# Kernel optimization log

Hardware: AMD Instinct MI355X
Metric: run time of the kernel (lower is better)

The kernel has to match this reference:

```python
import jax, jax.numpy as jnp
import numpy as np

S = 1024      # graphs (frames / LSTM seq_len)
NPG = 64      # nodes per graph
N = S * NPG   # total nodes
E = 524288    # total edges (512 per graph)
NF, EF = 32, 16
HC = 64       # hidden_channels
H1 = 3        # gat1 heads
NEG_SLOPE = 0.2


def _p(k, shape):
    return 0.1 * jax.random.normal(k, shape, dtype=jnp.float32)


def setup_inputs():
    key = jax.random.key(0)
    ks = jax.random.split(key, 30)
    x = jax.random.normal(ks[0], (N, NF), jnp.float32)
    local = jax.random.randint(ks[1], (2, E), 0, NPG)
    off = jnp.repeat(jnp.arange(S) * NPG, E // S)  # edges grouped per graph
    edge_index = local + off[None, :]
    edge_attr = jax.random.normal(ks[2], (E, EF), jnp.float32)
    batch = jnp.repeat(jnp.arange(S), NPG)
    return {
        'x': x, 'edge_index': edge_index, 'edge_attr': edge_attr, 'batch': batch,
        # gat1: in=NF, out=HC, heads=H1, edge_dim=EF
        'Wl1': _p(ks[3], (NF, H1 * HC)), 'bl1': _p(ks[4], (H1 * HC,)),
        'Wr1': _p(ks[5], (NF, H1 * HC)), 'br1': _p(ks[6], (H1 * HC,)),
        'We1': _p(ks[7], (EF, H1 * HC)), 'att1': _p(ks[8], (H1, HC)),
        'bias1': _p(ks[9], (H1 * HC,)),
        # gat2: in=H1*HC, out=HC, heads=1
        'Wl2': _p(ks[10], (H1 * HC, HC)), 'bl2': _p(ks[11], (HC,)),
        'Wr2': _p(ks[12], (H1 * HC, HC)), 'br2': _p(ks[13], (HC,)),
        'We2': _p(ks[14], (EF, HC)), 'att2': _p(ks[15], (1, HC)),
        'bias2': _p(ks[16], (HC,)),
        # LSTM (torch gate order i,f,g,o)
        'Wih': _p(ks[17], (4 * HC, HC)), 'Whh': _p(ks[18], (4 * HC, HC)),
        'bih': _p(ks[19], (4 * HC,)), 'bhh': _p(ks[20], (4 * HC,)),
        # MLP head
        'W1': _p(ks[21], (HC, HC // 2)), 'b1': _p(ks[22], (HC // 2,)),
        'W2': _p(ks[23], (HC // 2, 1)), 'b2': _p(ks[24], (1,)),
    }


def gatv2(x, edge_index, edge_attr, Wl, bl, Wr, br, We, att, bias, H, C):
    n = x.shape[0]
    src, dst = edge_index[0], edge_index[1]
    # add self loops, edge_attr filled with per-target mean (PyG fill_value='mean')
    deg = jax.ops.segment_sum(jnp.ones((edge_attr.shape[0],), x.dtype), dst, num_segments=n)
    loop_attr = jax.ops.segment_sum(edge_attr, dst, num_segments=n) / jnp.maximum(deg, 1.0)[:, None]
    ar = jnp.arange(n)
    src_f = jnp.concatenate([src, ar])
    dst_f = jnp.concatenate([dst, ar])
    ea_f = jnp.concatenate([edge_attr, loop_attr], axis=0)
    xl = (x @ Wl + bl).reshape(n, H, C)   # source-side transform (message carrier)
    xr = (x @ Wr + br).reshape(n, H, C)   # target-side transform
    eproj = (ea_f @ We).reshape(-1, H, C)
    m = jax.nn.leaky_relu(xl[src_f] + xr[dst_f] + eproj, NEG_SLOPE)  # [Ef,H,C]
    score = jnp.einsum('ehc,hc->eh', m, att)
    smax = jax.ops.segment_max(score, dst_f, num_segments=n)
    expv = jnp.exp(score - smax[dst_f])
    denom = jax.ops.segment_sum(expv, dst_f, num_segments=n)
    alpha = expv / (denom[dst_f] + 1e-16)
    out = jax.ops.segment_sum(alpha[..., None] * xl[src_f], dst_f, num_segments=n)
    return out.reshape(n, H * C) + bias


def lstm_last_hidden(seq, Wih, Whh, bih, bhh):
    # seq: [S, HC]; torch LSTM single layer, h0=c0=0
    def step(carry, xt):
        h, c = carry
        g = Wih @ xt + Whh @ h + bih + bhh
        i, f, gg, o = jnp.split(g, 4)
        c = jax.nn.sigmoid(f) * c + jax.nn.sigmoid(i) * jnp.tanh(gg)
        h = jax.nn.sigmoid(o) * jnp.tanh(c)
        return (h, c), None
    (h, c), _ = jax.lax.scan(step, (jnp.zeros((HC,), seq.dtype), jnp.zeros((HC,), seq.dtype)), seq)
    return h


def reference(x, edge_index, edge_attr, batch, Wl1, bl1, Wr1, br1, We1, att1, bias1,
              Wl2, bl2, Wr2, br2, We2, att2, bias2, Wih, Whh, bih, bhh, W1, b1, W2, b2):
    h = jax.nn.elu(gatv2(x, edge_index, edge_attr, Wl1, bl1, Wr1, br1, We1, att1, bias1, H1, HC))
    h = jax.nn.elu(gatv2(h, edge_index, edge_attr, Wl2, bl2, Wr2, br2, We2, att2, bias2, 1, HC))
    cnt = jax.ops.segment_sum(jnp.ones((N, 1), h.dtype), batch, num_segments=S)
    pooled = jax.ops.segment_sum(h, batch, num_segments=S) / cnt  # [S, HC]
    last = lstm_last_hidden(pooled, Wih, Whh, bih, bhh)[None, :]  # [1, HC]; dropout is identity in eval
    out = jax.nn.relu(last @ W1 + b1) @ W2 + b2  # [1, 1]
    return out
```

## Files before the change

### kernel.cpp

```cpp
#include <hip/hip_runtime.h>

#define ETOT 524288
#define SGR  1024
#define NPG  64
#define EPG  512
#define NFD  32
#define EFD  16
#define HCD  64

typedef float f2v __attribute__((ext_vector_type(2)));

__device__ __forceinline__ float elu_(float x){ return x>0.f ? x : (__expf(x)-1.f); }
__device__ __forceinline__ float sig_(float x){ return 1.f/(1.f+__expf(-x)); }
__device__ __forceinline__ float tanhf_(float x){ float e=__expf(2.f*x); return 1.f-2.f/(e+1.f); }
__device__ __forceinline__ float lrelu_(float x){ return x>0.f ? x : 0.2f*x; }

template<int C>
__device__ __forceinline__ float dppf(float v){
  return __int_as_float(__builtin_amdgcn_update_dpp(0, __float_as_int(v), C, 0xF, 0xF, true));
}

__device__ __forceinline__ float quad_add(float v){
  v += dppf<0xB1>(v);
  return v + dppf<0x4E>(v);
}

__device__ void build_csr_la(int tid, int g, const int* ei, const float* ea,
                             int* s_edge, int* s_entry, int* s_off, int* s_deg,
                             int* s_cnt, float* s_la)
{
  const int base = g*NPG;
  const int* srcp = ei + (size_t)g*EPG;
  const int* dstp = ei + (size_t)ETOT + (size_t)g*EPG;
  s_edge[tid] = (srcp[tid]-base) | ((dstp[tid]-base)<<6);
  __syncthreads();
  { const int d=tid>>3, s=tid&7, b0=s*64;
    int c=0;
    #pragma unroll 8
    for(int i=0;i<64;i++) c += (((s_edge[b0+i]>>6)&63)==d);
    s_cnt[(d<<3)|s]=c; }
  __syncthreads();
  if(tid<64){ int a=0;
    #pragma unroll
    for(int s=0;s<8;s++) a+=s_cnt[(tid<<3)|s];
    s_deg[tid]=a; }
  __syncthreads();
  if(tid==0){ int a=0;
    for(int i=0;i<64;i++){ s_off[i]=a; a+=s_deg[i]; }
    s_off[64]=a; }
  __syncthreads();
  { const int d=tid>>3, s=tid&7, b0=s*64;
    int pos=s_off[d];
    for(int s2=0;s2<s;s2++) pos += s_cnt[(d<<3)|s2];
    for(int i=0;i<64;i++){ int en=s_edge[b0+i];
      if(((en>>6)&63)==d) s_entry[pos++] = (en&63) | (d<<6) | ((b0+i)<<12); } }
  __syncthreads();
  if(tid<256){ int n=tid>>2, f0=(tid&3)*4;
    float a0=0,a1=0,a2=0,a3=0;
    const int b=s_off[n], en=s_off[n+1];
    for(int p=b;p<en;p++){ int eid=s_entry[p]>>12;
      const float4 v = *(const float4*)(ea + ((size_t)g*EPG+(size_t)eid)*EFD + f0);
      a0+=v.x; a1+=v.y; a2+=v.z; a3+=v.w; }
    float inv = 1.f/fmaxf((float)(en-b),1.f);
    float4 r; r.x=a0*inv; r.y=a1*inv; r.z=a2*inv; r.w=a3*inv;
    *(float4*)(s_la + n*EFD + f0) = r; }
  __syncthreads();
}

__device__ void scores_softmax(int tid, int g, const float* ea,
   const int* s_entry, const int* s_off, const float* s_la,
   const float* s_We, const float* s_att, const float* s_xl, const float* s_xr,
   float* s_sc)
{
  for(int p=tid;p<576;p+=512){
    int src,dst; float eav[16];
    if(p<EPG){
      int en=s_entry[p]; src=en&63; dst=(en>>6)&63; int eid=en>>12;
      const float* epp = ea + ((size_t)g*EPG + (size_t)eid)*EFD;
      float4 v0=*(const float4*)(epp),   v1=*(const float4*)(epp+4);
      float4 v2=*(const float4*)(epp+8), v3=*(const float4*)(epp+12);
      eav[0]=v0.x;eav[1]=v0.y;eav[2]=v0.z;eav[3]=v0.w;
      eav[4]=v1.x;eav[5]=v1.y;eav[6]=v1.z;eav[7]=v1.w;
      eav[8]=v2.x;eav[9]=v2.y;eav[10]=v2.z;eav[11]=v2.w;
      eav[12]=v3.x;eav[13]=v3.y;eav[14]=v3.z;eav[15]=v3.w;
    } else {
      int n=p-EPG; src=n; dst=n;
      const float* epp = s_la + n*EFD;
      float4 v0=*(const float4*)(epp),   v1=*(const float4*)(epp+4);
      float4 v2=*(const float4*)(epp+8), v3=*(const float4*)(epp+12);
      eav[0]=v0.x;eav[1]=v0.y;eav[2]=v0.z;eav[3]=v0.w;
      eav[4]=v1.x;eav[5]=v1.y;eav[6]=v1.z;eav[7]=v1.w;
      eav[8]=v2.x;eav[9]=v2.y;eav[10]=v2.z;eav[11]=v2.w;
      eav[12]=v3.x;eav[13]=v3.y;eav[14]=v3.z;eav[15]=v3.w;
    }
    float score=0.f;
    #pragma unroll 4
    for(int cq=0;cq<16;cq++){
      float e0=0.f,e1=0.f,e2=0.f,e3=0.f;
      #pragma unroll
      for(int f=0;f<16;f++){
        const float4 wv=*(const float4*)(s_We + f*64 + cq*4);
        e0+=eav[f]*wv.x; e1+=eav[f]*wv.y; e2+=eav[f]*wv.z; e3+=eav[f]*wv.w;
      }
      const float4 xlv=*(const float4*)(s_xl + src*64 + ((cq^(src&15))<<2));
      const float4 xrv=*(const float4*)(s_xr + dst*64 + ((cq^(dst&15))<<2));
      const float4 av =*(const float4*)(s_att + cq*4);
      float m0=lrelu_(xlv.x+xrv.x+e0), m1=lrelu_(xlv.y+xrv.y+e1);
      float m2=lrelu_(xlv.z+xrv.z+e2), m3=lrelu_(xlv.w+xrv.w+e3);
      score += m0*av.x+m1*av.y+m2*av.z+m3*av.w;
    }
    s_sc[p]=score;
  }
  __syncthreads();
  { const int d=tid>>3, s=tid&7;
    const int b=s_off[d], e=s_off[d+1];
    float mx=-1e30f;
    for(int p=b+s;p<e;p+=8) mx=fmaxf(mx,s_sc[p]);
    if(s==0) mx=fmaxf(mx,s_sc[EPG+d]);
    mx=fmaxf(mx,dppf<0xB1>(mx));
    mx=fmaxf(mx,dppf<0x4E>(mx));
    mx=fmaxf(mx,dppf<0x141>(mx));
    float den=0.f;
    for(int p=b+s;p<e;p+=8){ float w=__expf(s_sc[p]-mx); s_sc[p]=w; den+=w; }
    float selfv=0.f;
    if(s==0){ selfv=__expf(s_sc[EPG+d]-mx); den+=selfv; }
    den+=dppf<0xB1>(den);
    den+=dppf<0x4E>(den);
    den+=dppf<0x141>(den);
    const float inv=1.f/(den+1e-16f);
    for(int p=b+s;p<e;p+=8) s_sc[p]*=inv;
    if(s==0) s_sc[EPG+d]=selfv*inv;
  }
  __syncthreads();
}

__global__ __launch_bounds__(512,4) void gat1_k(
    const float* __restrict__ x, const int* __restrict__ ei,
    const float* __restrict__ ea, const float* __restrict__ Wl,
    const float* __restrict__ bl, const float* __restrict__ Wr,
    const float* __restrict__ br, const float* __restrict__ We,
    const float* __restrict__ att, const float* __restrict__ bias,
    float* __restrict__ h1)
{
  const int g = blockIdx.x, tid = threadIdx.x;
  const int base = g*NPG;

  __shared__ __align__(16) float s_x[NPG*36];
  __shared__ __align__(16) float s_xl[NPG*64];
  __shared__ __align__(16) float s_xr[NPG*64];
  __shared__ __align__(16) float s_W[2*32*64];
  __shared__ __align__(16) float s_We[16*64];
  __shared__ __align__(16) float s_att[64];
  __shared__ __align__(16) float s_la[NPG*EFD];
  __shared__ float s_sc[576];
  __shared__ int   s_edge[EPG];
  __shared__ int   s_entry[EPG];
  __shared__ int   s_cnt[512];
  __shared__ int   s_off[65];
  __shared__ int   s_deg[64];

  { int n=tid>>3, kq=tid&7;
    float4 v = *(const float4*)(x + (size_t)(base+n)*NFD + kq*4);
    *(float4*)(s_x + n*36 + kq*4) = v; }

  build_csr_la(tid, g, ei, ea, s_edge, s_entry, s_off, s_deg, s_cnt, s_la);

  for(int h=0;h<3;h++){
    { int k=tid>>4, c0=(tid&15)*4;
      *(float4*)(s_W + k*64 + c0)        = *(const float4*)(Wl + (size_t)k*192 + h*64 + c0);
      *(float4*)(s_W + 2048 + k*64 + c0) = *(const float4*)(Wr + (size_t)k*192 + h*64 + c0); }
    if(tid<256){ int f=tid>>4, c0=(tid&15)*4;
      *(float4*)(s_We + f*64 + c0) = *(const float4*)(We + (size_t)f*192 + h*64 + c0); }
    if(tid<16) *(float4*)(s_att + tid*4) = *(const float4*)(att + h*64 + tid*4);
    __syncthreads();

    { const int cg=tid&15, ng=tid>>4, n0=ng*2, c0=cg*4;
      const float4 blv=*(const float4*)(bl + h*64 + c0);
      const float4 brv=*(const float4*)(br + h*64 + c0);
      float accl[2][4]={{blv.x,blv.y,blv.z,blv.w},{blv.x,blv.y,blv.z,blv.w}};
      float accr[2][4]={{brv.x,brv.y,brv.z,brv.w},{brv.x,brv.y,brv.z,brv.w}};
      #pragma unroll
      for(int kq=0;kq<8;kq++){
        float xs0[4], xs1[4];
        { float4 v=*(const float4*)(s_x + n0*36 + kq*4);     xs0[0]=v.x;xs0[1]=v.y;xs0[2]=v.z;xs0[3]=v.w; }
        { float4 v=*(const float4*)(s_x + (n0+1)*36 + kq*4); xs1[0]=v.x;xs1[1]=v.y;xs1[2]=v.z;xs1[3]=v.w; }
        #pragma unroll
        for(int f=0;f<4;f++){
          const float4 wl=*(const float4*)(s_W + (kq*4+f)*64 + c0);
          const float4 wr=*(const float4*)(s_W + 2048 + (kq*4+f)*64 + c0);
          accl[0][0]+=xs0[f]*wl.x; accl[0][1]+=xs0[f]*wl.y; accl[0][2]+=xs0[f]*wl.z; accl[0][3]+=xs0[f]*wl.w;
          accl[1][0]+=xs1[f]*wl.x; accl[1][1]+=xs1[f]*wl.y; accl[1][2]+=xs1[f]*wl.z; accl[1][3]+=xs1[f]*wl.w;
          accr[0][0]+=xs0[f]*wr.x; accr[0][1]+=xs0[f]*wr.y; accr[0][2]+=xs0[f]*wr.z; accr[0][3]+=xs0[f]*wr.w;
          accr[1][0]+=xs1[f]*wr.x; accr[1][1]+=xs1[f]*wr.y; accr[1][2]+=xs1[f]*wr.z; accr[1][3]+=xs1[f]*wr.w;
        }
      }
      #pragma unroll
      for(int i=0;i<2;i++){
        const int n=n0+i, sq=((cg^(n&15))<<2);
        float4 vl; vl.x=accl[i][0]; vl.y=accl[i][1]; vl.z=accl[i][2]; vl.w=accl[i][3];
        float4 vr; vr.x=accr[i][0]; vr.y=accr[i][1]; vr.z=accr[i][2]; vr.w=accr[i][3];
        *(float4*)(s_xl + n*64 + sq)=vl;
        *(float4*)(s_xr + n*64 + sq)=vr;
      }
    }
    __syncthreads();

    scores_softmax(tid, g, ea, s_entry, s_off, s_la, s_We, s_att, s_xl, s_xr, s_sc);

    { const int n=tid>>3, c0a=(tid&7)*8;
      float acc[8]={0.f,0.f,0.f,0.f,0.f,0.f,0.f,0.f};
      const int b=s_off[n], e=s_off[n+1];
      for(int p=b;p<e;p++){
        const int en=s_entry[p], src=en&63;
        const float a=s_sc[p];
        #pragma unroll
        for(int qq=0;qq<2;qq++){
          const int cq=(c0a>>2)+qq;
          const float4 xv=*(const float4*)(s_xl + src*64 + ((cq^(src&15))<<2));
          acc[qq*4+0]+=a*xv.x; acc[qq*4+1]+=a*xv.y; acc[qq*4+2]+=a*xv.z; acc[qq*4+3]+=a*xv.w;
        }
      }
      { const float a=s_sc[EPG+n];
        #pragma unroll
        for(int qq=0;qq<2;qq++){
          const int cq=(c0a>>2)+qq;
          const float4 xv=*(const float4*)(s_xl + n*64 + ((cq^(n&15))<<2));
          acc[qq*4+0]+=a*xv.x; acc[qq*4+1]+=a*xv.y; acc[qq*4+2]+=a*xv.z; acc[qq*4+3]+=a*xv.w;
        } }
      float* op = h1 + (size_t)(base+n)*192 + h*64 + c0a;
      #pragma unroll
      for(int qq=0;qq<2;qq++){
        const float4 bv=*(const float4*)(bias + h*64 + c0a + qq*4);
        float4 r; r.x=elu_(acc[qq*4+0]+bv.x); r.y=elu_(acc[qq*4+1]+bv.y);
                  r.z=elu_(acc[qq*4+2]+bv.z); r.w=elu_(acc[qq*4+3]+bv.w);
        *(float4*)(op + qq*4)=r;
      }
    }
    __syncthreads();
  }
}

__global__ __launch_bounds__(512,4) void gat2_k(
    const float* __restrict__ h1, const int* __restrict__ ei,
    const float* __restrict__ ea, const float* __restrict__ Wl,
    const float* __restrict__ bl, const float* __restrict__ Wr,
    const float* __restrict__ br, const float* __restrict__ We,
    const float* __restrict__ att, const float* __restrict__ bias,
    const float* __restrict__ Wih, const float* __restrict__ bih,
    const float* __restrict__ bhh, float* __restrict__ xproj)
{
  const int g = blockIdx.x, tid = threadIdx.x;
  const int base = g*NPG;

  __shared__ __align__(16) float s_hx[NPG*36];
  __shared__ __align__(16) float s_xl[NPG*64];
  __shared__ __align__(16) float s_xr[NPG*64];
  __shared__ __align__(16) float s_W[2*32*64];
  __shared__ __align__(16) float s_We[16*64];
  __shared__ __align__(16) float s_att[64];
  __shared__ __align__(16) float s_la[NPG*EFD];
  __shared__ float s_sc[576];
  __shared__ float s_pool[64];
  __shared__ int   s_edge[EPG];
  __shared__ int   s_entry[EPG];
  __shared__ int   s_cnt[512];
  __shared__ int   s_off[65];
  __shared__ int   s_deg[64];
  float* s_out = s_W;

  build_csr_la(tid, g, ei, ea, s_edge, s_entry, s_off, s_deg, s_cnt, s_la);

  const int cg=tid&15, ng=tid>>4, n0=ng*2, gc0=cg*4;
  float accl[2][4], accr[2][4];
  { const float4 blv=*(const float4*)(bl + gc0);
    const float4 brv=*(const float4*)(br + gc0);
    #pragma unroll
    for(int i=0;i<2;i++){
      accl[i][0]=blv.x; accl[i][1]=blv.y; accl[i][2]=blv.z; accl[i][3]=blv.w;
      accr[i][0]=brv.x; accr[i][1]=brv.y; accr[i][2]=brv.z; accr[i][3]=brv.w; } }
  for(int kc=0;kc<6;kc++){
    { int n=tid>>3, kq=tid&7;
      *(float4*)(s_hx + n*36 + kq*4) = *(const float4*)(h1 + (size_t)(base+n)*192 + kc*32 + kq*4); }
    { int k=tid>>4, cc=(tid&15)*4;
      *(float4*)(s_W + k*64 + cc)        = *(const float4*)(Wl + (size_t)(kc*32+k)*64 + cc);
      *(float4*)(s_W + 2048 + k*64 + cc) = *(const float4*)(Wr + (size_t)(kc*32+k)*64 + cc); }
    __syncthreads();
    #pragma unroll
    for(int kq=0;kq<8;kq++){
      float xs0[4], xs1[4];
      { float4 v=*(const float4*)(s_hx + n0*36 + kq*4);     xs0[0]=v.x;xs0[1]=v.y;xs0[2]=v.z;xs0[3]=v.w; }
      { float4 v=*(const float4*)(s_hx + (n0+1)*36 + kq*4); xs1[0]=v.x;xs1[1]=v.y;xs1[2]=v.z;xs1[3]=v.w; }
      #pragma unroll
      for(int f=0;f<4;f++){
        const float4 wl=*(const float4*)(s_W + (kq*4+f)*64 + gc0);
        const float4 wr=*(const float4*)(s_W + 2048 + (kq*4+f)*64 + gc0);
        accl[0][0]+=xs0[f]*wl.x; accl[0][1]+=xs0[f]*wl.y; accl[0][2]+=xs0[f]*wl.z; accl[0][3]+=xs0[f]*wl.w;
        accl[1][0]+=xs1[f]*wl.x; accl[1][1]+=xs1[f]*wl.y; accl[1][2]+=xs1[f]*wl.z; accl[1][3]+=xs1[f]*wl.w;
        accr[0][0]+=xs0[f]*wr.x; accr[0][1]+=xs0[f]*wr.y; accr[0][2]+=xs0[f]*wr.z; accr[0][3]+=xs0[f]*wr.w;
        accr[1][0]+=xs1[f]*wr.x; accr[1][1]+=xs1[f]*wr.y; accr[1][2]+=xs1[f]*wr.z; accr[1][3]+=xs1[f]*wr.w;
      }
    }
    __syncthreads();
  }
  #pragma unroll
  for(int i=0;i<2;i++){
    const int n=n0+i, sq=((cg^(n&15))<<2);
    float4 vl; vl.x=accl[i][0]; vl.y=accl[i][1]; vl.z=accl[i][2]; vl.w=accl[i][3];
    float4 vr; vr.x=accr[i][0]; vr.y=accr[i][1]; vr.z=accr[i][2]; vr.w=accr[i][3];
    *(float4*)(s_xl + n*64 + sq)=vl;
    *(float4*)(s_xr + n*64 + sq)=vr;
  }
  if(tid<256){ int f=tid>>4, cc=(tid&15)*4;
    *(float4*)(s_We + f*64 + cc) = *(const float4*)(We + (size_t)f*64 + cc); }
  if(tid<16) *(float4*)(s_att + tid*4) = *(const float4*)(att + tid*4);
  __syncthreads();

  scores_softmax(tid, g, ea, s_entry, s_off, s_la, s_We, s_att, s_xl, s_xr, s_sc);

  { const int n=tid>>3, c0a=(tid&7)*8;
    float acc[8]={0.f,0.f,0.f,0.f,0.f,0.f,0.f,0.f};
    const int b=s_off[n], e=s_off[n+1];
    for(int p=b;p<e;p++){
      const int en=s_entry[p], src=en&63;
      const float a=s_sc[p];
      #pragma unroll
      for(int qq=0;qq<2;qq++){
        const int cq=(c0a>>2)+qq;
        const float4 xv=*(const float4*)(s_xl + src*64 + ((cq^(src&15))<<2));
        acc[qq*4+0]+=a*xv.x; acc[qq*4+1]+=a*xv.y; acc[qq*4+2]+=a*xv.z; acc[qq*4+3]+=a*xv.w;
      }
    }
    { const float a=s_sc[EPG+n];
      #pragma unroll
      for(int qq=0;qq<2;qq++){
        const int cq=(c0a>>2)+qq;
        const float4 xv=*(const float4*)(s_xl + n*64 + ((cq^(n&15))<<2));
        acc[qq*4+0]+=a*xv.x; acc[qq*4+1]+=a*xv.y; acc[qq*4+2]+=a*xv.z; acc[qq*4+3]+=a*xv.w;
      } }
    #pragma unroll
    for(int qq=0;qq<2;qq++){
      const float4 bv=*(const float4*)(bias + c0a + qq*4);
      float4 r; r.x=elu_(acc[qq*4+0]+bv.x); r.y=elu_(acc[qq*4+1]+bv.y);
                r.z=elu_(acc[qq*4+2]+bv.z); r.w=elu_(acc[qq*4+3]+bv.w);
      *(float4*)(s_out + n*64 + c0a + qq*4)=r;
    }
  }
  __syncthreads();
  if(tid<64){ float s=0.f;
    #pragma unroll 8
    for(int n2=0;n2<64;n2++) s += s_out[n2*64+tid];
    s_pool[tid]=s*(1.f/64.f); }
  __syncthreads();
  if(tid<256){
    float a=bih[tid]+bhh[tid];
    #pragma unroll
    for(int kq=0;kq<16;kq++){
      const float4 w=*(const float4*)(Wih + (size_t)tid*64 + kq*4);
      a += w.x*s_pool[kq*4+0] + w.y*s_pool[kq*4+1] + w.z*s_pool[kq*4+2] + w.w*s_pool[kq*4+3];
    }
    xproj[(size_t)g*256 + tid]=a;
  }
}

__device__ __forceinline__ float dot2_(f2v w0,f2v w1,f2v w2,f2v w3,f2v w4,f2v w5,f2v w6,f2v w7,
                                       f2v h0,f2v h1,f2v h2,f2v h3,f2v h4,f2v h5,f2v h6,f2v h7){
  f2v a = w0*h0; a += w1*h1; a += w2*h2; a += w3*h3;
  f2v b = w4*h4; b += w5*h5; b += w6*h6; b += w7*h7;
  f2v s = a+b; return s[0]+s[1];
}

#define WDECL(m) \
  f2v w##m##_0,w##m##_1,w##m##_2,w##m##_3,w##m##_4,w##m##_5,w##m##_6,w##m##_7; \
  { const float* wp_ = Whh + (size_t)((m)*64+l)*64 + q*16; \
    const float4 a_=*(const float4*)(wp_),   b_=*(const float4*)(wp_+4); \
    const float4 c_=*(const float4*)(wp_+8), d_=*(const float4*)(wp_+12); \
    w##m##_0=(f2v){a_.x,a_.y}; w##m##_1=(f2v){a_.z,a_.w}; \
    w##m##_2=(f2v){b_.x,b_.y}; w##m##_3=(f2v){b_.z,b_.w}; \
    w##m##_4=(f2v){c_.x,c_.y}; w##m##_5=(f2v){c_.z,c_.w}; \
    w##m##_6=(f2v){d_.x,d_.y}; w##m##_7=(f2v){d_.z,d_.w}; } \
  asm volatile("" : "+v"(w##m##_0),"+v"(w##m##_1),"+v"(w##m##_2),"+v"(w##m##_3), \
                    "+v"(w##m##_4),"+v"(w##m##_5),"+v"(w##m##_6),"+v"(w##m##_7));

#define DOTP(m) dot2_(w##m##_0,w##m##_1,w##m##_2,w##m##_3,w##m##_4,w##m##_5,w##m##_6,w##m##_7, \
                      hb0,hb1,hb2,hb3,hb4,hb5,hb6,hb7)

#define XQDECL(k) \
  float xq##k##_0,xq##k##_1,xq##k##_2,xq##k##_3; \
  { const float* xpp_ = xproj + (size_t)(k)*256; \
    xq##k##_0=xpp_[l]; xq##k##_1=xpp_[64+l]; xq##k##_2=xpp_[128+l]; xq##k##_3=xpp_[192+l]; }

#define STEP(k) { \
    f2v hb0,hb1,hb2,hb3,hb4,hb5,hb6,hb7; \
    { const float* hp_ = &s_h[cur][q*16]; \
      const float4 a_=*(const float4*)(hp_),   b_=*(const float4*)(hp_+4); \
      const float4 c_=*(const float4*)(hp_+8), d_=*(const float4*)(hp_+12); \
      hb0=(f2v){a_.x,a_.y}; hb1=(f2v){a_.z,a_.w}; \
      hb2=(f2v){b_.x,b_.y}; hb3=(f2v){b_.z,b_.w}; \
      hb4=(f2v){c_.x,c_.y}; hb5=(f2v){c_.z,c_.w}; \
      hb6=(f2v){d_.x,d_.y}; hb7=(f2v){d_.z,d_.w}; } \
    const float cx0=xq##k##_0, cx1=xq##k##_1, cx2=xq##k##_2, cx3=xq##k##_3; \
    if(tb+(k)+4<1024){ \
      const float* xpp_ = xproj + (size_t)(tb+(k)+4)*256; \
      xq##k##_0=xpp_[l]; xq##k##_1=xpp_[64+l]; xq##k##_2=xpp_[128+l]; xq##k##_3=xpp_[192+l]; \
    } \
    float a0=quad_add(DOTP(0)); \
    float a1=quad_add(DOTP(1)); \
    float a2=quad_add(DOTP(2)); \
    float a3=quad_add(DOTP(3)); \
    const float gi=a0+cx0, gf=a1+cx1, gg=a2+cx2, go=a3+cx3; \
    c = sig_(gf)*c + sig_(gi)*tanhf_(gg); \
    const float hn = sig_(go)*tanhf_(c); \
    if(q==0) s_h[cur^1][l]=hn; \
    cur^=1; \
    __syncthreads(); \
  }

__global__ __attribute__((amdgpu_flat_work_group_size(256,256), amdgpu_waves_per_eu(1,1)))
void lstm_k(
    const float* __restrict__ xproj, const float* __restrict__ Whh,
    const float* __restrict__ W1, const float* __restrict__ b1,
    const float* __restrict__ W2, const float* __restrict__ b2,
    float* __restrict__ out)
{
  const int tid=threadIdx.x, l=tid>>2, q=tid&3;
  __shared__ __align__(16) float s_h[2][64];
  __shared__ float s_y[32];

  WDECL(0) WDECL(1) WDECL(2) WDECL(3)
  XQDECL(0) XQDECL(1) XQDECL(2) XQDECL(3)

  float c=0.f;
  if(tid<64){ s_h[0][tid]=0.f; s_h[1][tid]=0.f; }
  __syncthreads();
  int cur=0;
  for(int tb=0;tb<1024;tb+=4){
    STEP(0) STEP(1) STEP(2) STEP(3)
  }
  if(tid<32){
    float a=b1[tid];
    #pragma unroll 8
    for(int k=0;k<64;k++) a += s_h[cur][k]*W1[k*32+tid];
    s_y[tid]=fmaxf(a,0.f);
  }
  __syncthreads();
  if(tid==0){
    float a=b2[0];
    #pragma unroll
    for(int j=0;j<32;j++) a += s_y[j]*W2[j];
    out[0]=a;
  }
}

extern "C" void kernel_launch(void* const* d_in, const int* in_sizes, int n_in,
                              void* d_out, int out_size, void* d_ws, size_t ws_size,
                              hipStream_t stream) {
  (void)in_sizes; (void)n_in; (void)out_size; (void)ws_size;
  const float* x    = (const float*)d_in[0];
  const int*   ei   = (const int*)d_in[1];
  const float* ea   = (const float*)d_in[2];
  const float* Wl1  = (const float*)d_in[4];
  const float* bl1  = (const float*)d_in[5];
  const float* Wr1  = (const float*)d_in[6];
  const float* br1  = (const float*)d_in[7];
  const float* We1  = (const float*)d_in[8];
  const float* att1 = (const float*)d_in[9];
  const float* bias1= (const float*)d_in[10];
  const float* Wl2  = (const float*)d_in[11];
  const float* bl2  = (const float*)d_in[12];
  const float* Wr2  = (const float*)d_in[13];
  const float* br2  = (const float*)d_in[14];
  const float* We2  = (const float*)d_in[15];
  const float* att2 = (const float*)d_in[16];
  const float* bias2= (const float*)d_in[17];
  const float* Wih  = (const float*)d_in[18];
  const float* Whh  = (const float*)d_in[19];
  const float* bih  = (const float*)d_in[20];
  const float* bhh  = (const float*)d_in[21];
  const float* W1   = (const float*)d_in[22];
  const float* b1   = (const float*)d_in[23];
  const float* W2   = (const float*)d_in[24];
  const float* b2   = (const float*)d_in[25];

  float* h1w = (float*)d_ws;
  float* xpw = (float*)((char*)d_ws + (size_t)50331648);
  float* outp = (float*)d_out;

  gat1_k<<<dim3(SGR), dim3(512), 0, stream>>>(x, ei, ea, Wl1, bl1, Wr1, br1, We1, att1, bias1, h1w);
  gat2_k<<<dim3(SGR), dim3(512), 0, stream>>>(h1w, ei, ea, Wl2, bl2, Wr2, br2, We2, att2, bias2,
                                              Wih, bih, bhh, xpw);
  lstm_k<<<dim3(1), dim3(256), 0, stream>>>(xpw, Whh, W1, b1, W2, b2, outp);
}
```

Before: 668.3 us.

## Fuse GAT layers and LSTM into one persistent kernel with flag-based streaming

Merges gat1, gat2 and the LSTM into a single launch. The layer-1 output stays in shared memory instead of being written to and re-read from global memory. Block 0 runs the sequential LSTM and spin-waits on per-graph release flags, so the recurrence can start while later graphs are still being computed by the other blocks. This removes the h1 round trip and two launch gaps. In exchange it adds a memset, relies on block 0 being co-resident with the producer blocks, and the larger shared-memory footprint may lower occupancy.

```diff
diff --git a/kernel.cpp b/kernel.cpp
--- a/kernel.cpp
+++ b/kernel.cpp
@@ -7,6 +7,7 @@
 #define NFD  32
 #define EFD  16
 #define HCD  64
+#define H1S  196
 
 typedef float f2v __attribute__((ext_vector_type(2)));
 
@@ -19,7 +20,6 @@
 __device__ __forceinline__ float dppf(float v){
   return __int_as_float(__builtin_amdgcn_update_dpp(0, __float_as_int(v), C, 0xF, 0xF, true));
 }
-
 __device__ __forceinline__ float quad_add(float v){
   v += dppf<0xB1>(v);
   return v + dppf<0x4E>(v);
@@ -134,234 +134,6 @@
   __syncthreads();
 }
 
-__global__ __launch_bounds__(512,4) void gat1_k(
-    const float* __restrict__ x, const int* __restrict__ ei,
-    const float* __restrict__ ea, const float* __restrict__ Wl,
-    const float* __restrict__ bl, const float* __restrict__ Wr,
-    const float* __restrict__ br, const float* __restrict__ We,
-    const float* __restrict__ att, const float* __restrict__ bias,
-    float* __restrict__ h1)
-{
-  const int g = blockIdx.x, tid = threadIdx.x;
-  const int base = g*NPG;
-
-  __shared__ __align__(16) float s_x[NPG*36];
-  __shared__ __align__(16) float s_xl[NPG*64];
-  __shared__ __align__(16) float s_xr[NPG*64];
-  __shared__ __align__(16) float s_W[2*32*64];
-  __shared__ __align__(16) float s_We[16*64];
-  __shared__ __align__(16) float s_att[64];
-  __shared__ __align__(16) float s_la[NPG*EFD];
-  __shared__ float s_sc[576];
-  __shared__ int   s_edge[EPG];
-  __shared__ int   s_entry[EPG];
-  __shared__ int   s_cnt[512];
-  __shared__ int   s_off[65];
-  __shared__ int   s_deg[64];
-
-  { int n=tid>>3, kq=tid&7;
-    float4 v = *(const float4*)(x + (size_t)(base+n)*NFD + kq*4);
-    *(float4*)(s_x + n*36 + kq*4) = v; }
-
-  build_csr_la(tid, g, ei, ea, s_edge, s_entry, s_off, s_deg, s_cnt, s_la);
-
-  for(int h=0;h<3;h++){
-    { int k=tid>>4, c0=(tid&15)*4;
-      *(float4*)(s_W + k*64 + c0)        = *(const float4*)(Wl + (size_t)k*192 + h*64 + c0);
-      *(float4*)(s_W + 2048 + k*64 + c0) = *(const float4*)(Wr + (size_t)k*192 + h*64 + c0); }
-    if(tid<256){ int f=tid>>4, c0=(tid&15)*4;
-      *(float4*)(s_We + f*64 + c0) = *(const float4*)(We + (size_t)f*192 + h*64 + c0); }
-    if(tid<16) *(float4*)(s_att + tid*4) = *(const float4*)(att + h*64 + tid*4);
-    __syncthreads();
-
-    { const int cg=tid&15, ng=tid>>4, n0=ng*2, c0=cg*4;
-      const float4 blv=*(const float4*)(bl + h*64 + c0);
-      const float4 brv=*(const float4*)(br + h*64 + c0);
-      float accl[2][4]={{blv.x,blv.y,blv.z,blv.w},{blv.x,blv.y,blv.z,blv.w}};
-      float accr[2][4]={{brv.x,brv.y,brv.z,brv.w},{brv.x,brv.y,brv.z,brv.w}};
-      #pragma unroll
-      for(int kq=0;kq<8;kq++){
-        float xs0[4], xs1[4];
-        { float4 v=*(const float4*)(s_x + n0*36 + kq*4);     xs0[0]=v.x;xs0[1]=v.y;xs0[2]=v.z;xs0[3]=v.w; }
-        { float4 v=*(const float4*)(s_x + (n0+1)*36 + kq*4); xs1[0]=v.x;xs1[1]=v.y;xs1[2]=v.z;xs1[3]=v.w; }
-        #pragma unroll
-        for(int f=0;f<4;f++){
-          const float4 wl=*(const float4*)(s_W + (kq*4+f)*64 + c0);
-          const float4 wr=*(const float4*)(s_W + 2048 + (kq*4+f)*64 + c0);
-          accl[0][0]+=xs0[f]*wl.x; accl[0][1]+=xs0[f]*wl.y; accl[0][2]+=xs0[f]*wl.z; accl[0][3]+=xs0[f]*wl.w;
-          accl[1][0]+=xs1[f]*wl.x; accl[1][1]+=xs1[f]*wl.y; accl[1][2]+=xs1[f]*wl.z; accl[1][3]+=xs1[f]*wl.w;
-          accr[0][0]+=xs0[f]*wr.x; accr[0][1]+=xs0[f]*wr.y; accr[0][2]+=xs0[f]*wr.z; accr[0][3]+=xs0[f]*wr.w;
-          accr[1][0]+=xs1[f]*wr.x; accr[1][1]+=xs1[f]*wr.y; accr[1][2]+=xs1[f]*wr.z; accr[1][3]+=xs1[f]*wr.w;
-        }
-      }
-      #pragma unroll
-      for(int i=0;i<2;i++){
-        const int n=n0+i, sq=((cg^(n&15))<<2);
-        float4 vl; vl.x=accl[i][0]; vl.y=accl[i][1]; vl.z=accl[i][2]; vl.w=accl[i][3];
-        float4 vr; vr.x=accr[i][0]; vr.y=accr[i][1]; vr.z=accr[i][2]; vr.w=accr[i][3];
-        *(float4*)(s_xl + n*64 + sq)=vl;
-        *(float4*)(s_xr + n*64 + sq)=vr;
-      }
-    }
-    __syncthreads();
-
-    scores_softmax(tid, g, ea, s_entry, s_off, s_la, s_We, s_att, s_xl, s_xr, s_sc);
-
-    { const int n=tid>>3, c0a=(tid&7)*8;
-      float acc[8]={0.f,0.f,0.f,0.f,0.f,0.f,0.f,0.f};
-      const int b=s_off[n], e=s_off[n+1];
-      for(int p=b;p<e;p++){
-        const int en=s_entry[p], src=en&63;
-        const float a=s_sc[p];
-        #pragma unroll
-        for(int qq=0;qq<2;qq++){
-          const int cq=(c0a>>2)+qq;
-          const float4 xv=*(const float4*)(s_xl + src*64 + ((cq^(src&15))<<2));
-          acc[qq*4+0]+=a*xv.x; acc[qq*4+1]+=a*xv.y; acc[qq*4+2]+=a*xv.z; acc[qq*4+3]+=a*xv.w;
-        }
-      }
-      { const float a=s_sc[EPG+n];
-        #pragma unroll
-        for(int qq=0;qq<2;qq++){
-          const int cq=(c0a>>2)+qq;
-          const float4 xv=*(const float4*)(s_xl + n*64 + ((cq^(n&15))<<2));
-          acc[qq*4+0]+=a*xv.x; acc[qq*4+1]+=a*xv.y; acc[qq*4+2]+=a*xv.z; acc[qq*4+3]+=a*xv.w;
-        } }
-      float* op = h1 + (size_t)(base+n)*192 + h*64 + c0a;
-      #pragma unroll
-      for(int qq=0;qq<2;qq++){
-        const float4 bv=*(const float4*)(bias + h*64 + c0a + qq*4);
-        float4 r; r.x=elu_(acc[qq*4+0]+bv.x); r.y=elu_(acc[qq*4+1]+bv.y);
-                  r.z=elu_(acc[qq*4+2]+bv.z); r.w=elu_(acc[qq*4+3]+bv.w);
-        *(float4*)(op + qq*4)=r;
-      }
-    }
-    __syncthreads();
-  }
-}
-
-__global__ __launch_bounds__(512,4) void gat2_k(
-    const float* __restrict__ h1, const int* __restrict__ ei,
-    const float* __restrict__ ea, const float* __restrict__ Wl,
-    const float* __restrict__ bl, const float* __restrict__ Wr,
-    const float* __restrict__ br, const float* __restrict__ We,
-    const float* __restrict__ att, const float* __restrict__ bias,
-    const float* __restrict__ Wih, const float* __restrict__ bih,
-    const float* __restrict__ bhh, float* __restrict__ xproj)
-{
-  const int g = blockIdx.x, tid = threadIdx.x;
-  const int base = g*NPG;
-
-  __shared__ __align__(16) float s_hx[NPG*36];
-  __shared__ __align__(16) float s_xl[NPG*64];
-  __shared__ __align__(16) float s_xr[NPG*64];
-  __shared__ __align__(16) float s_W[2*32*64];
-  __shared__ __align__(16) float s_We[16*64];
-  __shared__ __align__(16) float s_att[64];
-  __shared__ __align__(16) float s_la[NPG*EFD];
-  __shared__ float s_sc[576];
-  __shared__ float s_pool[64];
-  __shared__ int   s_edge[EPG];
-  __shared__ int   s_entry[EPG];
-  __shared__ int   s_cnt[512];
-  __shared__ int   s_off[65];
-  __shared__ int   s_deg[64];
-  float* s_out = s_W;
-
-  build_csr_la(tid, g, ei, ea, s_edge, s_entry, s_off, s_deg, s_cnt, s_la);
-
-  const int cg=tid&15, ng=tid>>4, n0=ng*2, gc0=cg*4;
-  float accl[2][4], accr[2][4];
-  { const float4 blv=*(const float4*)(bl + gc0);
-    const float4 brv=*(const float4*)(br + gc0);
-    #pragma unroll
-    for(int i=0;i<2;i++){
-      accl[i][0]=blv.x; accl[i][1]=blv.y; accl[i][2]=blv.z; accl[i][3]=blv.w;
-      accr[i][0]=brv.x; accr[i][1]=brv.y; accr[i][2]=brv.z; accr[i][3]=brv.w; } }
-  for(int kc=0;kc<6;kc++){
-    { int n=tid>>3, kq=tid&7;
-      *(float4*)(s_hx + n*36 + kq*4) = *(const float4*)(h1 + (size_t)(base+n)*192 + kc*32 + kq*4); }
-    { int k=tid>>4, cc=(tid&15)*4;
-      *(float4*)(s_W + k*64 + cc)        = *(const float4*)(Wl + (size_t)(kc*32+k)*64 + cc);
-      *(float4*)(s_W + 2048 + k*64 + cc) = *(const float4*)(Wr + (size_t)(kc*32+k)*64 + cc); }
-    __syncthreads();
-    #pragma unroll
-    for(int kq=0;kq<8;kq++){
-      float xs0[4], xs1[4];
-      { float4 v=*(const float4*)(s_hx + n0*36 + kq*4);     xs0[0]=v.x;xs0[1]=v.y;xs0[2]=v.z;xs0[3]=v.w; }
-      { float4 v=*(const float4*)(s_hx + (n0+1)*36 + kq*4); xs1[0]=v.x;xs1[1]=v.y;xs1[2]=v.z;xs1[3]=v.w; }
-      #pragma unroll
-      for(int f=0;f<4;f++){
-        const float4 wl=*(const float4*)(s_W + (kq*4+f)*64 + gc0);
-        const float4 wr=*(const float4*)(s_W + 2048 + (kq*4+f)*64 + gc0);
-        accl[0][0]+=xs0[f]*wl.x; accl[0][1]+=xs0[f]*wl.y; accl[0][2]+=xs0[f]*wl.z; accl[0][3]+=xs0[f]*wl.w;
-        accl[1][0]+=xs1[f]*wl.x; accl[1][1]+=xs1[f]*wl.y; accl[1][2]+=xs1[f]*wl.z; accl[1][3]+=xs1[f]*wl.w;
-        accr[0][0]+=xs0[f]*wr.x; accr[0][1]+=xs0[f]*wr.y; accr[0][2]+=xs0[f]*wr.z; accr[0][3]+=xs0[f]*wr.w;
-        accr[1][0]+=xs1[f]*wr.x; accr[1][1]+=xs1[f]*wr.y; accr[1][2]+=xs1[f]*wr.z; accr[1][3]+=xs1[f]*wr.w;
-      }
-    }
-    __syncthreads();
-  }
-  #pragma unroll
-  for(int i=0;i<2;i++){
-    const int n=n0+i, sq=((cg^(n&15))<<2);
-    float4 vl; vl.x=accl[i][0]; vl.y=accl[i][1]; vl.z=accl[i][2]; vl.w=accl[i][3];
-    float4 vr; vr.x=accr[i][0]; vr.y=accr[i][1]; vr.z=accr[i][2]; vr.w=accr[i][3];
-    *(float4*)(s_xl + n*64 + sq)=vl;
-    *(float4*)(s_xr + n*64 + sq)=vr;
-  }
-  if(tid<256){ int f=tid>>4, cc=(tid&15)*4;
-    *(float4*)(s_We + f*64 + cc) = *(const float4*)(We + (size_t)f*64 + cc); }
-  if(tid<16) *(float4*)(s_att + tid*4) = *(const float4*)(att + tid*4);
-  __syncthreads();
-
-  scores_softmax(tid, g, ea, s_entry, s_off, s_la, s_We, s_att, s_xl, s_xr, s_sc);
-
-  { const int n=tid>>3, c0a=(tid&7)*8;
-    float acc[8]={0.f,0.f,0.f,0.f,0.f,0.f,0.f,0.f};
-    const int b=s_off[n], e=s_off[n+1];
-    for(int p=b;p<e;p++){
-      const int en=s_entry[p], src=en&63;
-      const float a=s_sc[p];
-      #pragma unroll
-      for(int qq=0;qq<2;qq++){
-        const int cq=(c0a>>2)+qq;
-        const float4 xv=*(const float4*)(s_xl + src*64 + ((cq^(src&15))<<2));
-        acc[qq*4+0]+=a*xv.x; acc[qq*4+1]+=a*xv.y; acc[qq*4+2]+=a*xv.z; acc[qq*4+3]+=a*xv.w;
-      }
-    }
-    { const float a=s_sc[EPG+n];
-      #pragma unroll
-      for(int qq=0;qq<2;qq++){
-        const int cq=(c0a>>2)+qq;
-        const float4 xv=*(const float4*)(s_xl + n*64 + ((cq^(n&15))<<2));
-        acc[qq*4+0]+=a*xv.x; acc[qq*4+1]+=a*xv.y; acc[qq*4+2]+=a*xv.z; acc[qq*4+3]+=a*xv.w;
-      } }
-    #pragma unroll
-    for(int qq=0;qq<2;qq++){
-      const float4 bv=*(const float4*)(bias + c0a + qq*4);
-      float4 r; r.x=elu_(acc[qq*4+0]+bv.x); r.y=elu_(acc[qq*4+1]+bv.y);
-                r.z=elu_(acc[qq*4+2]+bv.z); r.w=elu_(acc[qq*4+3]+bv.w);
-      *(float4*)(s_out + n*64 + c0a + qq*4)=r;
-    }
-  }
-  __syncthreads();
-  if(tid<64){ float s=0.f;
-    #pragma unroll 8
-    for(int n2=0;n2<64;n2++) s += s_out[n2*64+tid];
-    s_pool[tid]=s*(1.f/64.f); }
-  __syncthreads();
-  if(tid<256){
-    float a=bih[tid]+bhh[tid];
-    #pragma unroll
-    for(int kq=0;kq<16;kq++){
-      const float4 w=*(const float4*)(Wih + (size_t)tid*64 + kq*4);
-      a += w.x*s_pool[kq*4+0] + w.y*s_pool[kq*4+1] + w.z*s_pool[kq*4+2] + w.w*s_pool[kq*4+3];
-    }
-    xproj[(size_t)g*256 + tid]=a;
-  }
-}
-
 __device__ __forceinline__ float dot2_(f2v w0,f2v w1,f2v w2,f2v w3,f2v w4,f2v w5,f2v w6,f2v w7,
                                        f2v h0,f2v h1,f2v h2,f2v h3,f2v h4,f2v h5,f2v h6,f2v h7){
   f2v a = w0*h0; a += w1*h1; a += w2*h2; a += w3*h3;
@@ -410,44 +182,259 @@
     const float gi=a0+cx0, gf=a1+cx1, gg=a2+cx2, go=a3+cx3; \
     c = sig_(gf)*c + sig_(gi)*tanhf_(gg); \
     const float hn = sig_(go)*tanhf_(c); \
-    if(q==0) s_h[cur^1][l]=hn; \
+    if(q==0 && tid<256) s_h[cur^1][l]=hn; \
     cur^=1; \
     __syncthreads(); \
   }
 
-__global__ __attribute__((amdgpu_flat_work_group_size(256,256), amdgpu_waves_per_eu(1,1)))
-void lstm_k(
-    const float* __restrict__ xproj, const float* __restrict__ Whh,
+__global__ __attribute__((amdgpu_flat_work_group_size(512,512), amdgpu_waves_per_eu(2,2)))
+void fused_k(
+    const float* __restrict__ x, const int* __restrict__ ei, const float* __restrict__ ea,
+    const float* __restrict__ Wl1, const float* __restrict__ bl1,
+    const float* __restrict__ Wr1, const float* __restrict__ br1,
+    const float* __restrict__ We1, const float* __restrict__ att1, const float* __restrict__ bias1,
+    const float* __restrict__ Wl2, const float* __restrict__ bl2,
+    const float* __restrict__ Wr2, const float* __restrict__ br2,
+    const float* __restrict__ We2, const float* __restrict__ att2, const float* __restrict__ bias2,
+    const float* __restrict__ Wih, const float* __restrict__ bih, const float* __restrict__ bhh,
+    const float* __restrict__ Whh,
     const float* __restrict__ W1, const float* __restrict__ b1,
     const float* __restrict__ W2, const float* __restrict__ b2,
-    float* __restrict__ out)
+    float* __restrict__ xproj, int* __restrict__ flags, float* __restrict__ out)
 {
-  const int tid=threadIdx.x, l=tid>>2, q=tid&3;
+  __shared__ __align__(16) float s_x[NPG*36];
+  __shared__ __align__(16) float s_h1[NPG*H1S];
+  __shared__ __align__(16) float s_xl[NPG*64];
+  __shared__ __align__(16) float s_xr[NPG*64];
+  __shared__ __align__(16) float s_W[2*32*64];
+  __shared__ __align__(16) float s_We[16*64];
+  __shared__ __align__(16) float s_att[64];
+  __shared__ __align__(16) float s_la[NPG*EFD];
+  __shared__ float s_sc[576];
+  __shared__ float s_pool[64];
+  __shared__ int   s_edge[EPG];
+  __shared__ int   s_entry[EPG];
+  __shared__ int   s_cnt[512];
+  __shared__ int   s_off[65];
+  __shared__ int   s_deg[64];
   __shared__ __align__(16) float s_h[2][64];
   __shared__ float s_y[32];
-
-  WDECL(0) WDECL(1) WDECL(2) WDECL(3)
-  XQDECL(0) XQDECL(1) XQDECL(2) XQDECL(3)
-
-  float c=0.f;
-  if(tid<64){ s_h[0][tid]=0.f; s_h[1][tid]=0.f; }
-  __syncthreads();
-  int cur=0;
-  for(int tb=0;tb<1024;tb+=4){
-    STEP(0) STEP(1) STEP(2) STEP(3)
-  }
-  if(tid<32){
-    float a=b1[tid];
+  __shared__ int   s_rd;
+
+  const int tid = threadIdx.x;
+
+  if(blockIdx.x == 0){
+    const int l=(tid>>2)&63, q=tid&3;
+    WDECL(0) WDECL(1) WDECL(2) WDECL(3)
+    float c=0.f;
+    if(tid<64){ s_h[0][tid]=0.f; s_h[1][tid]=0.f; }
+    if(tid==0) s_rd = -1;
+    __syncthreads();
+    if(tid==0){ int r=s_rd;
+      while(r<3){ while(__hip_atomic_load(&flags[r+1], __ATOMIC_ACQUIRE, __HIP_MEMORY_SCOPE_AGENT)==0){ __builtin_amdgcn_s_sleep(2); } r++; }
+      s_rd=r; }
+    __syncthreads();
+    XQDECL(0) XQDECL(1) XQDECL(2) XQDECL(3)
+    int cur=0;
+    for(int tb=0;tb<1024;tb+=4){
+      const int need = (tb+7<1023)?(tb+7):1023;
+      if(tid==0){ int r=s_rd;
+        while(r<need){ while(__hip_atomic_load(&flags[r+1], __ATOMIC_ACQUIRE, __HIP_MEMORY_SCOPE_AGENT)==0){ __builtin_amdgcn_s_sleep(2); } r++; }
+        s_rd=r; }
+      __syncthreads();
+      STEP(0) STEP(1) STEP(2) STEP(3)
+    }
+    if(tid<32){
+      float a=b1[tid];
+      #pragma unroll 8
+      for(int k=0;k<64;k++) a += s_h[cur][k]*W1[k*32+tid];
+      s_y[tid]=fmaxf(a,0.f);
+    }
+    __syncthreads();
+    if(tid==0){
+      float a=b2[0];
+      #pragma unroll
+      for(int j=0;j<32;j++) a += s_y[j]*W2[j];
+      out[0]=a;
+    }
+    return;
+  }
+
+  const int g = blockIdx.x - 1;
+  const int base = g*NPG;
+
+  { int n=tid>>3, kq=tid&7;
+    float4 v = *(const float4*)(x + (size_t)(base+n)*NFD + kq*4);
+    *(float4*)(s_x + n*36 + kq*4) = v; }
+
+  build_csr_la(tid, g, ei, ea, s_edge, s_entry, s_off, s_deg, s_cnt, s_la);
+
+  for(int h=0;h<3;h++){
+    { int k=tid>>4, c0=(tid&15)*4;
+      *(float4*)(s_W + k*64 + c0)        = *(const float4*)(Wl1 + (size_t)k*192 + h*64 + c0);
+      *(float4*)(s_W + 2048 + k*64 + c0) = *(const float4*)(Wr1 + (size_t)k*192 + h*64 + c0); }
+    if(tid<256){ int f=tid>>4, c0=(tid&15)*4;
+      *(float4*)(s_We + f*64 + c0) = *(const float4*)(We1 + (size_t)f*192 + h*64 + c0); }
+    if(tid<16) *(float4*)(s_att + tid*4) = *(const float4*)(att1 + h*64 + tid*4);
+    __syncthreads();
+
+    { const int cg=tid&15, ng=tid>>4, n0=ng*2, c0=cg*4;
+      const float4 blv=*(const float4*)(bl1 + h*64 + c0);
+      const float4 brv=*(const float4*)(br1 + h*64 + c0);
+      float accl[2][4]={{blv.x,blv.y,blv.z,blv.w},{blv.x,blv.y,blv.z,blv.w}};
+      float accr[2][4]={{brv.x,brv.y,brv.z,brv.w},{brv.x,brv.y,brv.z,brv.w}};
+      #pragma unroll
+      for(int kq=0;kq<8;kq++){
+        float xs0[4], xs1[4];
+        { float4 v=*(const float4*)(s_x + n0*36 + kq*4);     xs0[0]=v.x;xs0[1]=v.y;xs0[2]=v.z;xs0[3]=v.w; }
+        { float4 v=*(const float4*)(s_x + (n0+1)*36 + kq*4); xs1[0]=v.x;xs1[1]=v.y;xs1[2]=v.z;xs1[3]=v.w; }
+        #pragma unroll
+        for(int f=0;f<4;f++){
+          const float4 wl=*(const float4*)(s_W + (kq*4+f)*64 + c0);
+          const float4 wr=*(const float4*)(s_W + 2048 + (kq*4+f)*64 + c0);
+          accl[0][0]+=xs0[f]*wl.x; accl[0][1]+=xs0[f]*wl.y; accl[0][2]+=xs0[f]*wl.z; accl[0][3]+=xs0[f]*wl.w;
+          accl[1][0]+=xs1[f]*wl.x; accl[1][1]+=xs1[f]*wl.y; accl[1][2]+=xs1[f]*wl.z; accl[1][3]+=xs1[f]*wl.w;
+          accr[0][0]+=xs0[f]*wr.x; accr[0][1]+=xs0[f]*wr.y; accr[0][2]+=xs0[f]*wr.z; accr[0][3]+=xs0[f]*wr.w;
+          accr[1][0]+=xs1[f]*wr.x; accr[1][1]+=xs1[f]*wr.y; accr[1][2]+=xs1[f]*wr.z; accr[1][3]+=xs1[f]*wr.w;
+        }
+      }
+      #pragma unroll
+      for(int i=0;i<2;i++){
+        const int n=n0+i, sq=((cg^(n&15))<<2);
+        float4 vl; vl.x=accl[i][0]; vl.y=accl[i][1]; vl.z=accl[i][2]; vl.w=accl[i][3];
+        float4 vr; vr.x=accr[i][0]; vr.y=accr[i][1]; vr.z=accr[i][2]; vr.w=accr[i][3];
+        *(float4*)(s_xl + n*64 + sq)=vl;
+        *(float4*)(s_xr + n*64 + sq)=vr;
+      }
+    }
+    __syncthreads();
+
+    scores_softmax(tid, g, ea, s_entry, s_off, s_la, s_We, s_att, s_xl, s_xr, s_sc);
+
+    { const int n=tid>>3, c0a=(tid&7)*8;
+      float acc[8]={0.f,0.f,0.f,0.f,0.f,0.f,0.f,0.f};
+      const int b=s_off[n], e=s_off[n+1];
+      for(int p=b;p<e;p++){
+        const int en=s_entry[p], src=en&63;
+        const float a=s_sc[p];
+        #pragma unroll
+        for(int qq=0;qq<2;qq++){
+          const int cq=(c0a>>2)+qq;
+          const float4 xv=*(const float4*)(s_xl + src*64 + ((cq^(src&15))<<2));
+          acc[qq*4+0]+=a*xv.x; acc[qq*4+1]+=a*xv.y; acc[qq*4+2]+=a*xv.z; acc[qq*4+3]+=a*xv.w;
+        }
+      }
+      { const float a=s_sc[EPG+n];
+        #pragma unroll
+        for(int qq=0;qq<2;qq++){
+          const int cq=(c0a>>2)+qq;
+          const float4 xv=*(const float4*)(s_xl + n*64 + ((cq^(n&15))<<2));
+          acc[qq*4+0]+=a*xv.x; acc[qq*4+1]+=a*xv.y; acc[qq*4+2]+=a*xv.z; acc[qq*4+3]+=a*xv.w;
+        } }
+      #pragma unroll
+      for(int qq=0;qq<2;qq++){
+        const float4 bv=*(const float4*)(bias1 + h*64 + c0a + qq*4);
+        float4 r; r.x=elu_(acc[qq*4+0]+bv.x); r.y=elu_(acc[qq*4+1]+bv.y);
+                  r.z=elu_(acc[qq*4+2]+bv.z); r.w=elu_(acc[qq*4+3]+bv.w);
+        *(float4*)(s_h1 + n*H1S + h*64 + c0a + qq*4)=r;
+      }
+    }
+    __syncthreads();
+  }
+
+  const int cg=tid&15, ng=tid>>4, n0=ng*2, gc0=cg*4;
+  float accl[2][4], accr[2][4];
+  { const float4 blv=*(const float4*)(bl2 + gc0);
+    const float4 brv=*(const float4*)(br2 + gc0);
+    #pragma unroll
+    for(int i=0;i<2;i++){
+      accl[i][0]=blv.x; accl[i][1]=blv.y; accl[i][2]=blv.z; accl[i][3]=blv.w;
+      accr[i][0]=brv.x; accr[i][1]=brv.y; accr[i][2]=brv.z; accr[i][3]=brv.w; } }
+  for(int kc=0;kc<6;kc++){
+    { int k=tid>>4, cc=(tid&15)*4;
+      *(float4*)(s_W + k*64 + cc)        = *(const float4*)(Wl2 + (size_t)(kc*32+k)*64 + cc);
+      *(float4*)(s_W + 2048 + k*64 + cc) = *(const float4*)(Wr2 + (size_t)(kc*32+k)*64 + cc); }
+    __syncthreads();
+    #pragma unroll
+    for(int kq=0;kq<8;kq++){
+      float xs0[4], xs1[4];
+      { float4 v=*(const float4*)(s_h1 + n0*H1S + kc*32 + kq*4);     xs0[0]=v.x;xs0[1]=v.y;xs0[2]=v.z;xs0[3]=v.w; }
+      { float4 v=*(const float4*)(s_h1 + (n0+1)*H1S + kc*32 + kq*4); xs1[0]=v.x;xs1[1]=v.y;xs1[2]=v.z;xs1[3]=v.w; }
+      #pragma unroll
+      for(int f=0;f<4;f++){
+        const float4 wl=*(const float4*)(s_W + (kq*4+f)*64 + gc0);
+        const float4 wr=*(const float4*)(s_W + 2048 + (kq*4+f)*64 + gc0);
+        accl[0][0]+=xs0[f]*wl.x; accl[0][1]+=xs0[f]*wl.y; accl[0][2]+=xs0[f]*wl.z; accl[0][3]+=xs0[f]*wl.w;
+        accl[1][0]+=xs1[f]*wl.x; accl[1][1]+=xs1[f]*wl.y; accl[1][2]+=xs1[f]*wl.z; accl[1][3]+=xs1[f]*wl.w;
+        accr[0][0]+=xs0[f]*wr.x; accr[0][1]+=xs0[f]*wr.y; accr[0][2]+=xs0[f]*wr.z; accr[0][3]+=xs0[f]*wr.w;
+        accr[1][0]+=xs1[f]*wr.x; accr[1][1]+=xs1[f]*wr.y; accr[1][2]+=xs1[f]*wr.z; accr[1][3]+=xs1[f]*wr.w;
+      }
+    }
+    __syncthreads();
+  }
+  #pragma unroll
+  for(int i=0;i<2;i++){
+    const int n=n0+i, sq=((cg^(n&15))<<2);
+    float4 vl; vl.x=accl[i][0]; vl.y=accl[i][1]; vl.z=accl[i][2]; vl.w=accl[i][3];
+    float4 vr; vr.x=accr[i][0]; vr.y=accr[i][1]; vr.z=accr[i][2]; vr.w=accr[i][3];
+    *(float4*)(s_xl + n*64 + sq)=vl;
+    *(float4*)(s_xr + n*64 + sq)=vr;
+  }
+  if(tid<256){ int f=tid>>4, cc=(tid&15)*4;
+    *(float4*)(s_We + f*64 + cc) = *(const float4*)(We2 + (size_t)f*64 + cc); }
+  if(tid<16) *(float4*)(s_att + tid*4) = *(const float4*)(att2 + tid*4);
+  __syncthreads();
+
+  scores_softmax(tid, g, ea, s_entry, s_off, s_la, s_We, s_att, s_xl, s_xr, s_sc);
+
+  float* s_out = s_W;
+  { const int n=tid>>3, c0a=(tid&7)*8;
+    float acc[8]={0.f,0.f,0.f,0.f,0.f,0.f,0.f,0.f};
+    const int b=s_off[n], e=s_off[n+1];
+    for(int p=b;p<e;p++){
+      const int en=s_entry[p], src=en&63;
+      const float a=s_sc[p];
+      #pragma unroll
+      for(int qq=0;qq<2;qq++){
+        const int cq=(c0a>>2)+qq;
+        const float4 xv=*(const float4*)(s_xl + src*64 + ((cq^(src&15))<<2));
+        acc[qq*4+0]+=a*xv.x; acc[qq*4+1]+=a*xv.y; acc[qq*4+2]+=a*xv.z; acc[qq*4+3]+=a*xv.w;
+      }
+    }
+    { const float a=s_sc[EPG+n];
+      #pragma unroll
+      for(int qq=0;qq<2;qq++){
+        const int cq=(c0a>>2)+qq;
+        const float4 xv=*(const float4*)(s_xl + n*64 + ((cq^(n&15))<<2));
+        acc[qq*4+0]+=a*xv.x; acc[qq*4+1]+=a*xv.y; acc[qq*4+2]+=a*xv.z; acc[qq*4+3]+=a*xv.w;
+      } }
+    #pragma unroll
+    for(int qq=0;qq<2;qq++){
+      const float4 bv=*(const float4*)(bias2 + c0a + qq*4);
+      float4 r; r.x=elu_(acc[qq*4+0]+bv.x); r.y=elu_(acc[qq*4+1]+bv.y);
+                r.z=elu_(acc[qq*4+2]+bv.z); r.w=elu_(acc[qq*4+3]+bv.w);
+      *(float4*)(s_out + n*64 + c0a + qq*4)=r;
+    }
+  }
+  __syncthreads();
+  if(tid<64){ float s=0.f;
     #pragma unroll 8
-    for(int k=0;k<64;k++) a += s_h[cur][k]*W1[k*32+tid];
-    s_y[tid]=fmaxf(a,0.f);
+    for(int n2=0;n2<64;n2++) s += s_out[n2*64+tid];
+    s_pool[tid]=s*(1.f/64.f); }
+  __syncthreads();
+  if(tid<256){
+    float a=bih[tid]+bhh[tid];
+    #pragma unroll
+    for(int kq=0;kq<16;kq++){
+      const float4 w=*(const float4*)(Wih + (size_t)tid*64 + kq*4);
+      a += w.x*s_pool[kq*4+0] + w.y*s_pool[kq*4+1] + w.z*s_pool[kq*4+2] + w.w*s_pool[kq*4+3];
+    }
+    xproj[(size_t)g*256 + tid]=a;
   }
   __syncthreads();
   if(tid==0){
-    float a=b2[0];
-    #pragma unroll
-    for(int j=0;j<32;j++) a += s_y[j]*W2[j];
-    out[0]=a;
+    __threadfence();
+    __hip_atomic_store(&flags[g], 1, __ATOMIC_RELEASE, __HIP_MEMORY_SCOPE_AGENT);
   }
 }
 
@@ -481,12 +468,14 @@
   const float* W2   = (const float*)d_in[24];
   const float* b2   = (const float*)d_in[25];
 
-  float* h1w = (float*)d_ws;
-  float* xpw = (float*)((char*)d_ws + (size_t)50331648);
-  float* outp = (float*)d_out;
-
-  gat1_k<<<dim3(SGR), dim3(512), 0, stream>>>(x, ei, ea, Wl1, bl1, Wr1, br1, We1, att1, bias1, h1w);
-  gat2_k<<<dim3(SGR), dim3(512), 0, stream>>>(h1w, ei, ea, Wl2, bl2, Wr2, br2, We2, att2, bias2,
-                                              Wih, bih, bhh, xpw);
-  lstm_k<<<dim3(1), dim3(256), 0, stream>>>(xpw, Whh, W1, b1, W2, b2, outp);
-}
+  float* xpw   = (float*)d_ws;
+  int*   flags = (int*)((char*)d_ws + (size_t)1048576);
+  float* outp  = (float*)d_out;
+
+  hipMemsetAsync(flags, 0, 1024*sizeof(int), stream);
+  fused_k<<<dim3(SGR+1), dim3(512), 0, stream>>>(
+      x, ei, ea, Wl1, bl1, Wr1, br1, We1, att1, bias1,
+      Wl2, bl2, Wr2, br2, We2, att2, bias2,
+      Wih, bih, bhh, Whh, W1, b1, W2, b2,
+      xpw, flags, outp);
+}
```

Result: slower. 823.2 us (+23.2%).
